# Optimization experiments

Measured on AMD Instinct MI355X. Metric: run time of the kernel, lower is better.

Reference implementation:

```python
import jax, jax.numpy as jnp
import numpy as np

B, S, I, E, NH, HID, L = 32, 512, 64, 128, 8, 1024, 4
HD = E // NH
TEMP = 0.05
EPS_BN = 1e-5
EPS_LN = 1e-5


def _pe(seq_len, d_model):
    # sinusoidal positional encoding, matches PositionalEncoding buffer pe[:seq_len, 0, :]
    pos = jnp.arange(seq_len, dtype=jnp.float32)[:, None]
    div = jnp.exp(jnp.arange(0, d_model, 2, dtype=jnp.float32) * (-np.log(10000.0) / d_model))
    pe = jnp.zeros((seq_len, d_model), jnp.float32)
    pe = pe.at[:, 0::2].set(jnp.sin(pos * div))
    pe = pe.at[:, 1::2].set(jnp.cos(pos * div))
    return pe


def _bn(x, g, b, axis):
    # eval-mode BatchNorm1d with running_mean=0, running_var=1 (affine scale+shift)
    sh = [1] * x.ndim
    sh[axis] = -1
    return x * (g / jnp.sqrt(1.0 + EPS_BN)).reshape(sh) + b.reshape(sh)


def _ln(x, g, b):
    m = jnp.mean(x, axis=-1, keepdims=True)
    v = jnp.var(x, axis=-1, keepdims=True)
    return (x - m) / jnp.sqrt(v + EPS_LN) * g + b


def _layer(h, Wqkv, bqkv, Wo, bo, g1, b1, g2, b2, W1, bf1, W2, bf2):
    # h: (S, B, E); post-LN torch TransformerEncoderLayer, relu FFN
    s, b = h.shape[0], h.shape[1]
    qkv = h @ Wqkv + bqkv                                  # (S, B, 3E)
    q, k, v = jnp.split(qkv, 3, axis=-1)
    sp = lambda t: t.reshape(s, b, NH, HD).transpose(1, 2, 0, 3)  # (B, NH, S, HD)
    q, k, v = sp(q), sp(k), sp(v)
    att = jax.nn.softmax(jnp.einsum('bhqd,bhkd->bhqk', q, k) * (1.0 / np.sqrt(HD)), axis=-1)
    o = jnp.einsum('bhqk,bhkd->bhqd', att, v).transpose(2, 0, 1, 3).reshape(s, b, E)
    h = _ln(h + o @ Wo + bo, g1, b1)
    ff = jax.nn.relu(h @ W1 + bf1) @ W2 + bf2
    h = _ln(h + ff, g2, b2)
    return h, att.mean(axis=1)  # attn averaged over heads: (B, S, S)


def setup_inputs() -> dict:
    key = jax.random.key(0)
    ks = iter(jax.random.split(key, 64))
    r = lambda *sh: jax.random.normal(next(ks), sh, jnp.float32) * 0.02
    return dict(
        x=jax.random.normal(next(ks), (B, S, I), jnp.float32),
        Wt=r(I, E), bt=r(E),
        bn1_g=jnp.ones(E), bn1_b=jnp.zeros(E),
        bn2_g=jnp.ones(E), bn2_b=jnp.zeros(E),
        Wqkv=r(L, E, 3 * E), bqkv=r(L, 3 * E), Wo=r(L, E, E), bo=r(L, E),
        ln1_g=jnp.ones((L, E)), ln1_b=jnp.zeros((L, E)),
        ln2_g=jnp.ones((L, E)), ln2_b=jnp.zeros((L, E)),
        W1=r(L, E, HID), b1=r(L, HID), W2=r(L, HID, E), b2=r(L, E),
        bn3_g=jnp.ones(E), bn3_b=jnp.zeros(E),
        Wd=r(E, I), bd=r(I), bn4_g=jnp.ones(I), bn4_b=jnp.zeros(I),
        Ws=r(S, HID), bs=r(HID), bn5_g=jnp.ones(HID), bn5_b=jnp.zeros(HID),
        Wtext=r(1024, HID), btext=r(HID), lnT_g=jnp.ones(HID), lnT_b=jnp.zeros(HID),
        sensor_emb=jax.random.normal(next(ks), (I, 1024), jnp.float32),
    )


def reference(x, Wt, bt, bn1_g, bn1_b, bn2_g, bn2_b,
              Wqkv, bqkv, Wo, bo, ln1_g, ln1_b, ln2_g, ln2_b,
              W1, b1, W2, b2, bn3_g, bn3_b,
              Wd, bd, bn4_g, bn4_b, Ws, bs, bn5_g, bn5_b,
              Wtext, btext, lnT_g, lnT_b, sensor_emb):
    # trunk_net: Linear -> BN(E) -> PE -> BN(E)
    h = x @ Wt + bt                                  # (B, S, E)
    h = _bn(h.transpose(0, 2, 1), bn1_g, bn1_b, 1)   # (B, E, S)
    h = h.transpose(2, 0, 1)                         # (S, B, E)
    h = h + _pe(h.shape[0], E)[:, None, :]
    h = _bn(h.transpose(1, 2, 0), bn2_g, bn2_b, 1)   # (B, E, S)
    h = h.transpose(2, 0, 1)                         # (S, B, E)
    for i in range(L):
        h, attn = _layer(h, Wqkv[i], bqkv[i], Wo[i], bo[i],
                         ln1_g[i], ln1_b[i], ln2_g[i], ln2_b[i],
                         W1[i], b1[i], W2[i], b2[i])
    h = _bn(h.transpose(1, 2, 0), bn3_g, bn3_b, 1)   # (B, E, S)
    # downsample_embedding_to_input_net
    d = jax.nn.relu(h.transpose(0, 2, 1) @ Wd + bd)  # (B, S, I)
    d = _bn(d.transpose(0, 2, 1), bn4_g, bn4_b, 1)   # (B, I, S)
    # sequence_representation_net
    imu = jax.nn.relu(d @ Ws + bs)                   # (B, I, HID)
    imu = _bn(imu, bn5_g, bn5_b, 2)
    # text_to_shared_net on sensor embeddings
    sens = _ln(jax.nn.relu(sensor_emb @ Wtext + btext), lnT_g, lnT_b)  # (I, HID)
    # fused pairwise cosine similarity (torch expands to (B,I,I,HID); we don't)
    imu_n = imu / jnp.maximum(jnp.linalg.norm(imu, axis=-1, keepdims=True), 1e-8)
    sens_n = sens / jnp.maximum(jnp.linalg.norm(sens, axis=-1, keepdims=True), 1e-8)
    return jnp.einsum('bih,jh->bij', imu_n, sens_n) / TEMP  # (B, I, I)
```

## Files before the change

kernel.cpp:

```cpp
#include <hip/hip_runtime.h>
#include <hip/hip_bf16.h>

#define B_   32
#define S_   512
#define I_   64
#define E_   128
#define NH_  8
#define HD_  16
#define HID_ 1024
#define L_   4
#define NTOK (B_*S_)

typedef __hip_bfloat16 bf16;
typedef __attribute__((ext_vector_type(8))) short bf16x8;
typedef __attribute__((ext_vector_type(4))) float f32x4;

__device__ __forceinline__ float b2f(bf16 v) { return __bfloat162float(v); }

template<bool F32>
__device__ __forceinline__ float ld(const void* p, size_t i) {
    if (F32) return ((const float*)p)[i];
    return b2f(((const bf16*)p)[i]);
}

__device__ __forceinline__ unsigned short f2bu(float f) {
    union { bf16 h; unsigned short u; } c; c.h = __float2bfloat16(f); return c.u;
}
__device__ __forceinline__ unsigned short b2u(bf16 h) {
    union { bf16 h; unsigned short u; } c; c.h = h; return c.u;
}

__global__ void k_flag(const void* bn1g, int* flag) {
    if (threadIdx.x == 0) {
        const unsigned short* u = (const unsigned short*)bn1g;
        int zeros = 0;
        for (int i = 0; i < 32; ++i) zeros += (u[i] == 0);
        flag[0] = (zeros >= 8) ? 1 : 0;
    }
}

template<bool F32>
__device__ void tr_body(const void* in, bf16* __restrict__ out, int R, int C,
                        float (*tile)[33])
{
    size_t off = (size_t)blockIdx.z * R * C;
    int c0 = blockIdx.x * 32, r0 = blockIdx.y * 32;
    int tx = threadIdx.x;
    for (int i = threadIdx.y; i < 32; i += 8)
        tile[i][tx] = ld<F32>(in, off + (size_t)(r0 + i) * C + c0 + tx);
    __syncthreads();
    for (int i = threadIdx.y; i < 32; i += 8)
        out[off + (size_t)(c0 + i) * R + r0 + tx] = __float2bfloat16(tile[tx][i]);
}
__global__ __launch_bounds__(256) void k_tr(
    const void* in, bf16* out, int R, int C, const int* flag)
{
    __shared__ float tile[32][33];
    if (*flag) tr_body<true>(in, out, R, C, tile);
    else       tr_body<false>(in, out, R, C, tile);
}

template<bool F32>
__device__ void trunk_body(const void* x, const void* Wt, const void* bt,
                           const void* g1, const void* c1,
                           const void* g2, const void* c2, float* __restrict__ h,
                           float (*xs)[I_])
{
    const int TOK = 8;
    int t0 = blockIdx.x * TOK;
    int tid = threadIdx.x;
    for (int idx = tid; idx < TOK * I_; idx += 128) {
        int tt = idx >> 6, k = idx & 63;
        xs[tt][k] = ld<F32>(x, (size_t)(t0 + tt) * I_ + k);
    }
    __syncthreads();
    int e = tid;
    float acc[TOK];
    float bias = ld<F32>(bt, e);
#pragma unroll
    for (int tt = 0; tt < TOK; ++tt) acc[tt] = bias;
    for (int k = 0; k < I_; ++k) {
        float w = ld<F32>(Wt, k * E_ + e);
#pragma unroll
        for (int tt = 0; tt < TOK; ++tt) acc[tt] += xs[tt][k] * w;
    }
    float rs = rsqrtf(1.0f + 1e-5f);
    float a1 = ld<F32>(g1, e) * rs, d1 = ld<F32>(c1, e);
    float a2 = ld<F32>(g2, e) * rs, d2 = ld<F32>(c2, e);
    int p = e >> 1;
    float freq = __expf(-(float)p * 0.14391157f);
#pragma unroll
    for (int tt = 0; tt < TOK; ++tt) {
        int t = t0 + tt;
        int s = t & (S_ - 1);
        float ang = (float)s * freq;
        float pe = (e & 1) ? cosf(ang) : sinf(ang);
        float v = acc[tt] * a1 + d1 + pe;
        h[(size_t)t * E_ + e] = v * a2 + d2;
    }
}
__global__ __launch_bounds__(128) void k_trunk(
    const void* x, const void* Wt, const void* bt,
    const void* g1, const void* c1, const void* g2, const void* c2,
    float* h, const int* flag)
{
    __shared__ float xs[8][I_];
    if (*flag) trunk_body<true>(x, Wt, bt, g1, c1, g2, c2, h, xs);
    else       trunk_body<false>(x, Wt, bt, g1, c1, g2, c2, h, xs);
}

template<bool F32>
__device__ void qkvm_body(const float* __restrict__ h, const bf16* __restrict__ WT,
                          const void* bias, size_t obi, bf16* __restrict__ qkv,
                          unsigned short (*A_s)[136])
{
    int t0 = blockIdx.x * 32;
    int tid = threadIdx.x;
    int wv = tid >> 6, lane = tid & 63;
    int l15 = lane & 15, quad = lane >> 4;

    {
        const float4* h4 = (const float4*)(h + (size_t)t0 * E_);
        for (int i = tid; i < 32 * E_ / 4; i += 256) {
            float4 v = h4[i];
            int row = i >> 5, col = (i & 31) * 4;
            A_s[row][col + 0] = f2bu(v.x);
            A_s[row][col + 1] = f2bu(v.y);
            A_s[row][col + 2] = f2bu(v.z);
            A_s[row][col + 3] = f2bu(v.w);
        }
    }
    __syncthreads();

    bf16x8 af[2][4];
#pragma unroll
    for (int kt = 0; kt < 4; ++kt) {
        int k0 = kt * 32 + quad * 8;
        af[0][kt] = *(const bf16x8*)&A_s[l15][k0];
        af[1][kt] = *(const bf16x8*)&A_s[16 + l15][k0];
    }
    for (int nt = 0; nt < 6; ++nt) {
        int col = wv * 96 + nt * 16 + l15;
        f32x4 acc0 = {0.f, 0.f, 0.f, 0.f}, acc1 = {0.f, 0.f, 0.f, 0.f};
#pragma unroll
        for (int kt = 0; kt < 4; ++kt) {
            bf16x8 bfr = *(const bf16x8*)&WT[(size_t)col * E_ + kt * 32 + quad * 8];
            acc0 = __builtin_amdgcn_mfma_f32_16x16x32_bf16(af[0][kt], bfr, acc0, 0, 0, 0);
            acc1 = __builtin_amdgcn_mfma_f32_16x16x32_bf16(af[1][kt], bfr, acc1, 0, 0, 0);
        }
        float bb = ld<F32>(bias, obi + col);
#pragma unroll
        for (int r = 0; r < 4; ++r) {
            qkv[(size_t)(t0 + quad * 4 + r) * 384 + col]      = __float2bfloat16(acc0[r] + bb);
            qkv[(size_t)(t0 + 16 + quad * 4 + r) * 384 + col] = __float2bfloat16(acc1[r] + bb);
        }
    }
}
__global__ __launch_bounds__(256) void k_qkv(
    const float* h, const bf16* WT, const void* bias, size_t obi,
    bf16* qkv, const int* flag)
{
    __shared__ unsigned short A_s[32][136];
    if (*flag) qkvm_body<true>(h, WT, bias, obi, qkv, A_s);
    else       qkvm_body<false>(h, WT, bias, obi, qkv, A_s);
}

__global__ __launch_bounds__(256) void k_attn(bf16* qkv)
{
    __shared__ unsigned short Qs[64 * 24];
    __shared__ unsigned short Ks[S_ * 24];
    __shared__ unsigned short VT[HD_ * 520];
    __shared__ unsigned short Pb[4][16 * 40];

    int bx = blockIdx.x;
    int qg = bx & 7;
    int hh = (bx >> 3) & (NH_ - 1);
    int b  = bx >> 6;
    int tid = threadIdx.x;
    const size_t base = (size_t)(b * S_) * 384 + hh * HD_;
    const float qscale = 0.25f * 1.44269504f;

    for (int i = tid; i < S_ * 8; i += 256) {
        int d2 = i & 7, s = i >> 3;
        const bf16* row = qkv + base + (size_t)s * 384;
        unsigned int uk = (unsigned int)b2u(row[128 + 2 * d2])
                        | ((unsigned int)b2u(row[128 + 2 * d2 + 1]) << 16);
        ((unsigned int*)Ks)[s * 12 + d2] = uk;
    }
    for (int i = tid; i < 64 * 8; i += 256) {
        int d2 = i & 7, s = i >> 3;
        const bf16* row = qkv + base + (size_t)(qg * 64 + s) * 384;
        unsigned int uq = (unsigned int)f2bu(b2f(row[2 * d2]) * qscale)
                        | ((unsigned int)f2bu(b2f(row[2 * d2 + 1]) * qscale) << 16);
        ((unsigned int*)Qs)[s * 12 + d2] = uq;
    }
    for (int i = tid; i < HD_ * (S_ / 2); i += 256) {
        int d = i & 15, s2 = i >> 4;
        unsigned int uv = (unsigned int)b2u(qkv[base + (size_t)(2 * s2) * 384 + 256 + d])
                        | ((unsigned int)b2u(qkv[base + (size_t)(2 * s2 + 1) * 384 + 256 + d]) << 16);
        ((unsigned int*)VT)[d * 260 + s2] = uv;
    }
    __syncthreads();

    int wv = tid >> 6, lane = tid & 63;
    int l15 = lane & 15, quad = lane >> 4;
    bool loquad = (quad < 2);
    unsigned short* Pw = &Pb[wv][0];
    const f32x4 z4 = {0.f, 0.f, 0.f, 0.f};

    bf16x8 B1 = {0, 0, 0, 0, 0, 0, 0, 0};
    if (loquad) B1 = *(const bf16x8*)&Qs[(wv * 16 + l15) * 24 + quad * 8];

    float den = 0.f;
    f32x4 O = z4;

    for (int kt2 = 0; kt2 < 16; ++kt2) {
        int key0 = kt2 * 32;
        bf16x8 A1a = {0, 0, 0, 0, 0, 0, 0, 0};
        bf16x8 A1b = {0, 0, 0, 0, 0, 0, 0, 0};
        if (loquad) {
            A1a = *(const bf16x8*)&Ks[(key0 + l15) * 24 + quad * 8];
            A1b = *(const bf16x8*)&Ks[(key0 + 16 + l15) * 24 + quad * 8];
        }
        f32x4 S1 = __builtin_amdgcn_mfma_f32_16x16x32_bf16(A1a, B1, z4, 0, 0, 0);
        f32x4 S2 = __builtin_amdgcn_mfma_f32_16x16x32_bf16(A1b, B1, z4, 0, 0, 0);

        float p[8];
#pragma unroll
        for (int r = 0; r < 4; ++r) { p[r] = exp2f(S1[r]); den += p[r]; }
#pragma unroll
        for (int r = 0; r < 4; ++r) { p[4 + r] = exp2f(S2[r]); den += p[4 + r]; }

        unsigned int w0 = (unsigned int)f2bu(p[0]) | ((unsigned int)f2bu(p[1]) << 16);
        unsigned int w1 = (unsigned int)f2bu(p[2]) | ((unsigned int)f2bu(p[3]) << 16);
        *(uint2*)&Pw[l15 * 40 + quad * 4] = (uint2){w0, w1};
        unsigned int w2 = (unsigned int)f2bu(p[4]) | ((unsigned int)f2bu(p[5]) << 16);
        unsigned int w3 = (unsigned int)f2bu(p[6]) | ((unsigned int)f2bu(p[7]) << 16);
        *(uint2*)&Pw[l15 * 40 + 16 + quad * 4] = (uint2){w2, w3};

        bf16x8 A2 = *(const bf16x8*)&Pw[l15 * 40 + quad * 8];
        bf16x8 B2 = *(const bf16x8*)&VT[l15 * 520 + key0 + quad * 8];
        O = __builtin_amdgcn_mfma_f32_16x16x32_bf16(A2, B2, O, 0, 0, 0);
    }

    den += __shfl_xor(den, 16, 64);
    den += __shfl_xor(den, 32, 64);
    float inv = 1.0f / den;
    int q0 = qg * 64 + wv * 16;
#pragma unroll
    for (int r = 0; r < 4; ++r) {
        float oi = O[r] * __shfl(inv, quad * 4 + r, 64);
        qkv[(size_t)(b * S_ + q0 + quad * 4 + r) * 384 + hh * HD_ + l15] =
            __float2bfloat16(oi);
    }
}

template<bool F32>
__device__ void projm_body(const bf16* __restrict__ qkv, const bf16* __restrict__ WoT,
                           const void* bo, size_t obo,
                           const void* g, const void* be, size_t oln,
                           float* __restrict__ h,
                           unsigned short (*A_s)[136], float (*red)[32][2])
{
    int t0 = blockIdx.x * 32;
    int tid = threadIdx.x;
    int wv = tid >> 6, lane = tid & 63;
    int l15 = lane & 15, quad = lane >> 4;

    for (int i = tid; i < 32 * 16; i += 256) {
        int row = i >> 4, seg = i & 15;
        *(uint4*)&A_s[row][seg * 8] =
            *(const uint4*)&qkv[(size_t)(t0 + row) * 384 + seg * 8];
    }
    __syncthreads();

    bf16x8 af[2][4];
#pragma unroll
    for (int kt = 0; kt < 4; ++kt) {
        int k0 = kt * 32 + quad * 8;
        af[0][kt] = *(const bf16x8*)&A_s[l15][k0];
        af[1][kt] = *(const bf16x8*)&A_s[16 + l15][k0];
    }
    f32x4 acc[2][2];
#pragma unroll
    for (int a = 0; a < 2; ++a)
#pragma unroll
        for (int bn = 0; bn < 2; ++bn) acc[a][bn] = (f32x4){0.f, 0.f, 0.f, 0.f};
    int c0 = wv * 32 + l15, c1 = c0 + 16;
#pragma unroll
    for (int kt = 0; kt < 4; ++kt) {
        int k0 = kt * 32 + quad * 8;
        bf16x8 bb0 = *(const bf16x8*)&WoT[(size_t)c0 * E_ + k0];
        bf16x8 bb1 = *(const bf16x8*)&WoT[(size_t)c1 * E_ + k0];
        acc[0][0] = __builtin_amdgcn_mfma_f32_16x16x32_bf16(af[0][kt], bb0, acc[0][0], 0, 0, 0);
        acc[1][0] = __builtin_amdgcn_mfma_f32_16x16x32_bf16(af[1][kt], bb0, acc[1][0], 0, 0, 0);
        acc[0][1] = __builtin_amdgcn_mfma_f32_16x16x32_bf16(af[0][kt], bb1, acc[0][1], 0, 0, 0);
        acc[1][1] = __builtin_amdgcn_mfma_f32_16x16x32_bf16(af[1][kt], bb1, acc[1][1], 0, 0, 0);
    }

    float bo0 = ld<F32>(bo, obo + c0), bo1 = ld<F32>(bo, obo + c1);
    float val[2][2][4], s1[2][4], s2[2][4];
#pragma unroll
    for (int mt = 0; mt < 2; ++mt) {
#pragma unroll
        for (int r = 0; r < 4; ++r) {
            size_t row = (size_t)(t0 + mt * 16 + quad * 4 + r);
            float v0 = acc[mt][0][r] + bo0 + h[row * E_ + c0];
            float v1 = acc[mt][1][r] + bo1 + h[row * E_ + c1];
            val[mt][0][r] = v0; val[mt][1][r] = v1;
            s1[mt][r] = v0 + v1;
            s2[mt][r] = v0 * v0 + v1 * v1;
        }
    }
#pragma unroll
    for (int off = 1; off < 16; off <<= 1) {
#pragma unroll
        for (int mt = 0; mt < 2; ++mt)
#pragma unroll
            for (int r = 0; r < 4; ++r) {
                s1[mt][r] += __shfl_xor(s1[mt][r], off, 64);
                s2[mt][r] += __shfl_xor(s2[mt][r], off, 64);
            }
    }
    if (l15 == 0) {
#pragma unroll
        for (int mt = 0; mt < 2; ++mt)
#pragma unroll
            for (int r = 0; r < 4; ++r) {
                red[wv][mt * 16 + quad * 4 + r][0] = s1[mt][r];
                red[wv][mt * 16 + quad * 4 + r][1] = s2[mt][r];
            }
    }
    __syncthreads();
    float g0 = ld<F32>(g, oln + c0), g1v = ld<F32>(g, oln + c1);
    float be0 = ld<F32>(be, oln + c0), be1 = ld<F32>(be, oln + c1);
#pragma unroll
    for (int mt = 0; mt < 2; ++mt) {
#pragma unroll
        for (int r = 0; r < 4; ++r) {
            int rw = mt * 16 + quad * 4 + r;
            float su = red[0][rw][0] + red[1][rw][0] + red[2][rw][0] + red[3][rw][0];
            float sq = red[0][rw][1] + red[1][rw][1] + red[2][rw][1] + red[3][rw][1];
            float mean = su * (1.0f / E_);
            float var = fmaxf(sq * (1.0f / E_) - mean * mean, 0.0f);
            float rstd = rsqrtf(var + 1e-5f);
            size_t row = (size_t)(t0 + rw);
            h[row * E_ + c0] = (val[mt][0][r] - mean) * rstd * g0 + be0;
            h[row * E_ + c1] = (val[mt][1][r] - mean) * rstd * g1v + be1;
        }
    }
}
__global__ __launch_bounds__(256) void k_proj(
    const bf16* qkv, const bf16* WoT, const void* bo, size_t obo,
    const void* g, const void* be, size_t oln, float* h, const int* flag)
{
    __shared__ unsigned short A_s[32][136];
    __shared__ float red[4][32][2];
    if (*flag) projm_body<true>(qkv, WoT, bo, obo, g, be, oln, h, A_s, red);
    else       projm_body<false>(qkv, WoT, bo, obo, g, be, oln, h, A_s, red);
}

#define FTOK 32
#define APAD 8
#define MPAD 8

template<bool F32>
__device__ void ffn_body(float* __restrict__ h,
                         const bf16* __restrict__ W1T, const void* b1, size_t ob1,
                         const bf16* __restrict__ W2T, const void* b2v, size_t ob2,
                         const void* g, const void* be, size_t oln,
                         unsigned short (*A_s)[E_ + APAD],
                         unsigned short (*mid_s)[HID_ + MPAD],
                         float (*red)[32][2])
{
    int t0 = blockIdx.x * FTOK;
    int tid = threadIdx.x;
    int wv = tid >> 6, lane = tid & 63;
    int l15 = lane & 15, quad = lane >> 4;

    {
        const float4* h4 = (const float4*)(h + (size_t)t0 * E_);
        for (int i = tid; i < FTOK * E_ / 4; i += 256) {
            float4 v = h4[i];
            int row = i >> 5, col = (i & 31) * 4;
            A_s[row][col + 0] = f2bu(v.x);
            A_s[row][col + 1] = f2bu(v.y);
            A_s[row][col + 2] = f2bu(v.z);
            A_s[row][col + 3] = f2bu(v.w);
        }
    }
    __syncthreads();

    {
        bf16x8 af[2][4];
#pragma unroll
        for (int kt = 0; kt < 4; ++kt) {
            int k0 = kt * 32 + quad * 8;
            af[0][kt] = *(const bf16x8*)&A_s[l15][k0];
            af[1][kt] = *(const bf16x8*)&A_s[16 + l15][k0];
        }
        for (int nt = 0; nt < 16; ++nt) {
            int col = wv * 256 + nt * 16 + l15;
            f32x4 acc0 = {0.f, 0.f, 0.f, 0.f}, acc1 = {0.f, 0.f, 0.f, 0.f};
#pragma unroll
            for (int kt = 0; kt < 4; ++kt) {
                bf16x8 bfr = *(const bf16x8*)&W1T[(size_t)col * E_ + kt * 32 + quad * 8];
                acc0 = __builtin_amdgcn_mfma_f32_16x16x32_bf16(af[0][kt], bfr, acc0, 0, 0, 0);
                acc1 = __builtin_amdgcn_mfma_f32_16x16x32_bf16(af[1][kt], bfr, acc1, 0, 0, 0);
            }
            float bias = ld<F32>(b1, ob1 + col);
#pragma unroll
            for (int r = 0; r < 4; ++r) {
                mid_s[quad * 4 + r][col]      = f2bu(fmaxf(acc0[r] + bias, 0.f));
                mid_s[16 + quad * 4 + r][col] = f2bu(fmaxf(acc1[r] + bias, 0.f));
            }
        }
    }
    __syncthreads();

    f32x4 acc[2][2];
#pragma unroll
    for (int a = 0; a < 2; ++a)
#pragma unroll
        for (int bn = 0; bn < 2; ++bn) acc[a][bn] = (f32x4){0.f, 0.f, 0.f, 0.f};
    int c0 = wv * 32 + l15;
    int c1 = wv * 32 + 16 + l15;
    for (int kt = 0; kt < 32; ++kt) {
        int k0 = kt * 32 + quad * 8;
        bf16x8 a0 = *(const bf16x8*)&mid_s[l15][k0];
        bf16x8 a1 = *(const bf16x8*)&mid_s[16 + l15][k0];
        bf16x8 bb0 = *(const bf16x8*)&W2T[(size_t)c0 * HID_ + k0];
        bf16x8 bb1 = *(const bf16x8*)&W2T[(size_t)c1 * HID_ + k0];
        acc[0][0] = __builtin_amdgcn_mfma_f32_16x16x32_bf16(a0, bb0, acc[0][0], 0, 0, 0);
        acc[1][0] = __builtin_amdgcn_mfma_f32_16x16x32_bf16(a1, bb0, acc[1][0], 0, 0, 0);
        acc[0][1] = __builtin_amdgcn_mfma_f32_16x16x32_bf16(a0, bb1, acc[0][1], 0, 0, 0);
        acc[1][1] = __builtin_amdgcn_mfma_f32_16x16x32_bf16(a1, bb1, acc[1][1], 0, 0, 0);
    }

    float bo0 = ld<F32>(b2v, ob2 + c0), bo1 = ld<F32>(b2v, ob2 + c1);
    float val[2][2][4], s1[2][4], s2[2][4];
#pragma unroll
    for (int mt = 0; mt < 2; ++mt) {
#pragma unroll
        for (int r = 0; r < 4; ++r) {
            size_t row = (size_t)(t0 + mt * 16 + quad * 4 + r);
            float v0 = acc[mt][0][r] + bo0 + h[row * E_ + c0];
            float v1 = acc[mt][1][r] + bo1 + h[row * E_ + c1];
            val[mt][0][r] = v0; val[mt][1][r] = v1;
            s1[mt][r] = v0 + v1;
            s2[mt][r] = v0 * v0 + v1 * v1;
        }
    }
#pragma unroll
    for (int off = 1; off < 16; off <<= 1) {
#pragma unroll
        for (int mt = 0; mt < 2; ++mt)
#pragma unroll
            for (int r = 0; r < 4; ++r) {
                s1[mt][r] += __shfl_xor(s1[mt][r], off, 64);
                s2[mt][r] += __shfl_xor(s2[mt][r], off, 64);
            }
    }
    if (l15 == 0) {
#pragma unroll
        for (int mt = 0; mt < 2; ++mt)
#pragma unroll
            for (int r = 0; r < 4; ++r) {
                red[wv][mt * 16 + quad * 4 + r][0] = s1[mt][r];
                red[wv][mt * 16 + quad * 4 + r][1] = s2[mt][r];
            }
    }
    __syncthreads();
    float g0 = ld<F32>(g, oln + c0), g1v = ld<F32>(g, oln + c1);
    float be0 = ld<F32>(be, oln + c0), be1 = ld<F32>(be, oln + c1);
#pragma unroll
    for (int mt = 0; mt < 2; ++mt) {
#pragma unroll
        for (int r = 0; r < 4; ++r) {
            int rw = mt * 16 + quad * 4 + r;
            float su = red[0][rw][0] + red[1][rw][0] + red[2][rw][0] + red[3][rw][0];
            float sq = red[0][rw][1] + red[1][rw][1] + red[2][rw][1] + red[3][rw][1];
            float mean = su * (1.0f / E_);
            float var = fmaxf(sq * (1.0f / E_) - mean * mean, 0.0f);
            float rstd = rsqrtf(var + 1e-5f);
            size_t row = (size_t)(t0 + rw);
            h[row * E_ + c0] = (val[mt][0][r] - mean) * rstd * g0 + be0;
            h[row * E_ + c1] = (val[mt][1][r] - mean) * rstd * g1v + be1;
        }
    }
}
__global__ __launch_bounds__(256) void k_ffn_mfma(
    float* h, const bf16* W1T, const void* b1, size_t ob1,
    const bf16* W2T, const void* b2v, size_t ob2,
    const void* g, const void* be, size_t oln, const int* flag)
{
    __shared__ unsigned short A_s[FTOK][E_ + APAD];
    __shared__ unsigned short mid_s[FTOK][HID_ + MPAD];
    __shared__ float red[4][32][2];
    if (*flag) ffn_body<true>(h, W1T, b1, ob1, W2T, b2v, ob2, g, be, oln, A_s, mid_s, red);
    else       ffn_body<false>(h, W1T, b1, ob1, W2T, b2v, ob2, g, be, oln, A_s, mid_s, red);
}

template<bool F32>
__device__ void downm_body(const float* __restrict__ h, const void* g3, const void* c3,
                           const bf16* __restrict__ WdT, const void* bd,
                           const void* g4, const void* c4, float* __restrict__ d,
                           unsigned short (*A_s)[136], float* g3s, float* c3s)
{
    int t0 = blockIdx.x * 32;
    int tid = threadIdx.x;
    if (tid < E_) {
        float rs = rsqrtf(1.0f + 1e-5f);
        g3s[tid] = ld<F32>(g3, tid) * rs;
        c3s[tid] = ld<F32>(c3, tid);
    }
    __syncthreads();
    for (int i = tid; i < 32 * E_; i += 256) {
        int row = i >> 7, col = i & 127;
        A_s[row][col] = f2bu(h[(size_t)(t0 + row) * E_ + col] * g3s[col] + c3s[col]);
    }
    __syncthreads();

    int wv = tid >> 6, lane = tid & 63;
    int l15 = lane & 15, quad = lane >> 4;
    int col = wv * 16 + l15;
    f32x4 acc0 = {0.f, 0.f, 0.f, 0.f}, acc1 = {0.f, 0.f, 0.f, 0.f};
#pragma unroll
    for (int kt = 0; kt < 4; ++kt) {
        int k0 = kt * 32 + quad * 8;
        bf16x8 a0 = *(const bf16x8*)&A_s[l15][k0];
        bf16x8 a1 = *(const bf16x8*)&A_s[16 + l15][k0];
        bf16x8 bb = *(const bf16x8*)&WdT[(size_t)col * E_ + k0];
        acc0 = __builtin_amdgcn_mfma_f32_16x16x32_bf16(a0, bb, acc0, 0, 0, 0);
        acc1 = __builtin_amdgcn_mfma_f32_16x16x32_bf16(a1, bb, acc1, 0, 0, 0);
    }
    float rs = rsqrtf(1.0f + 1e-5f);
    float bb = ld<F32>(bd, col);
    float a4 = ld<F32>(g4, col) * rs, d4 = ld<F32>(c4, col);
#pragma unroll
    for (int r = 0; r < 4; ++r) {
        d[(size_t)(t0 + quad * 4 + r) * I_ + col]      = fmaxf(acc0[r] + bb, 0.f) * a4 + d4;
        d[(size_t)(t0 + 16 + quad * 4 + r) * I_ + col] = fmaxf(acc1[r] + bb, 0.f) * a4 + d4;
    }
}
__global__ __launch_bounds__(256) void k_down(
    const float* h, const void* g3, const void* c3, const bf16* WdT, const void* bd,
    const void* g4, const void* c4, float* d, const int* flag)
{
    __shared__ unsigned short A_s[32][136];
    __shared__ float g3s[E_], c3s[E_];
    if (*flag) downm_body<true>(h, g3, c3, WdT, bd, g4, c4, d, A_s, g3s, c3s);
    else       downm_body<false>(h, g3, c3, WdT, bd, g4, c4, d, A_s, g3s, c3s);
}

template<bool F32>
__device__ void imum_body(const float* __restrict__ d, const bf16* __restrict__ WsT,
                          const void* bs, const void* g5, const void* c5,
                          float* __restrict__ imu, unsigned short (*A_s)[520])
{
    int b = blockIdx.x >> 3;
    int jc = blockIdx.x & 7;
    int tid = threadIdx.x;
    int wv = tid >> 6, lane = tid & 63;
    int l15 = lane & 15, quad = lane >> 4;

    for (int idx = tid; idx < I_ * S_; idx += 256) {
        int i = idx & 63, s = idx >> 6;
        A_s[i][s] = f2bu(d[((size_t)b * S_ + s) * I_ + i]);
    }
    __syncthreads();

    float rs = rsqrtf(1.0f + 1e-5f);
    int j0 = jc * 128 + wv * 32;
    for (int nt = 0; nt < 2; ++nt) {
        int j = j0 + nt * 16 + l15;
        f32x4 acc4[4];
#pragma unroll
        for (int mt = 0; mt < 4; ++mt) acc4[mt] = (f32x4){0.f, 0.f, 0.f, 0.f};
        for (int kt = 0; kt < 16; ++kt) {
            int k0 = kt * 32 + quad * 8;
            bf16x8 bfr = *(const bf16x8*)&WsT[(size_t)j * S_ + k0];
#pragma unroll
            for (int mt = 0; mt < 4; ++mt) {
                bf16x8 a = *(const bf16x8*)&A_s[mt * 16 + l15][k0];
                acc4[mt] = __builtin_amdgcn_mfma_f32_16x16x32_bf16(a, bfr, acc4[mt], 0, 0, 0);
            }
        }
        float bias = ld<F32>(bs, j);
        float a5 = ld<F32>(g5, j) * rs, d5 = ld<F32>(c5, j);
#pragma unroll
        for (int mt = 0; mt < 4; ++mt) {
#pragma unroll
            for (int r = 0; r < 4; ++r) {
                int row = mt * 16 + quad * 4 + r;
                float v = fmaxf(acc4[mt][r] + bias, 0.f) * a5 + d5;
                imu[((size_t)b * I_ + row) * HID_ + j] = v;
            }
        }
    }
}
__global__ __launch_bounds__(256) void k_imu(
    const float* d, const bf16* WsT, const void* bs,
    const void* g5, const void* c5, float* imu, const int* flag)
{
    __shared__ unsigned short A_s[I_][520];
    if (*flag) imum_body<true>(d, WsT, bs, g5, c5, imu, A_s);
    else       imum_body<false>(d, WsT, bs, g5, c5, imu, A_s);
}

__global__ __launch_bounds__(256) void k_norm(float* __restrict__ imu)
{
    __shared__ float red[4];
    size_t r0 = (size_t)blockIdx.x * HID_;
    int tid = threadIdx.x;
    float sq = 0.f;
    for (int k = tid; k < HID_; k += 256) { float v = imu[r0 + k]; sq += v * v; }
    for (int off = 32; off; off >>= 1) sq += __shfl_down(sq, off, 64);
    int wv = tid >> 6, lane = tid & 63;
    if (lane == 0) red[wv] = sq;
    __syncthreads();
    float tot = red[0] + red[1] + red[2] + red[3];
    float inv = 1.0f / fmaxf(sqrtf(fmaxf(tot, 0.f)), 1e-8f);
    for (int k = tid; k < HID_; k += 256) imu[r0 + k] *= inv;
}

template<bool F32>
__device__ void sensg_body(const void* se, const bf16* __restrict__ WtT,
                           const void* bt, float* __restrict__ sg,
                           unsigned short (*A_s)[HID_ + 8])
{
    int mt = blockIdx.x >> 4;
    int nc = blockIdx.x & 15;
    int r0 = mt * 16;
    int tid = threadIdx.x;
    int wv = tid >> 6, lane = tid & 63;
    int l15 = lane & 15, quad = lane >> 4;

    for (int i = tid; i < 16 * HID_; i += 256) {
        int row = i >> 10, col = i & (HID_ - 1);
        A_s[row][col] = f2bu(ld<F32>(se, (size_t)(r0 + row) * HID_ + col));
    }
    __syncthreads();

    int col = nc * 64 + wv * 16 + l15;
    f32x4 acc = {0.f, 0.f, 0.f, 0.f};
    for (int kt = 0; kt < 32; ++kt) {
        int k0 = kt * 32 + quad * 8;
        bf16x8 a = *(const bf16x8*)&A_s[l15][k0];
        bf16x8 bb = *(const bf16x8*)&WtT[(size_t)col * HID_ + k0];
        acc = __builtin_amdgcn_mfma_f32_16x16x32_bf16(a, bb, acc, 0, 0, 0);
    }
    float bbv = ld<F32>(bt, col);
#pragma unroll
    for (int r = 0; r < 4; ++r)
        sg[(size_t)(r0 + quad * 4 + r) * HID_ + col] = fmaxf(acc[r] + bbv, 0.f);
}
__global__ __launch_bounds__(256) void k_sens_gemm(
    const void* se, const bf16* WtT, const void* bt, float* sg, const int* flag)
{
    __shared__ unsigned short A_s[16][HID_ + 8];
    if (*flag) sensg_body<true>(se, WtT, bt, sg, A_s);
    else       sensg_body<false>(se, WtT, bt, sg, A_s);
}

template<bool F32>
__device__ void sensln_body(const float* __restrict__ sg, const void* g, const void* be,
                            bf16* __restrict__ sens_b, float (*red)[2])
{
    size_t r0 = (size_t)blockIdx.x * HID_;
    int tid = threadIdx.x;
    int wv = tid >> 6, lane = tid & 63;
    float v4[4];
    float s1 = 0.f, s2 = 0.f;
#pragma unroll
    for (int c = 0; c < 4; ++c) {
        float v = sg[r0 + tid + c * 256];
        v4[c] = v;
        s1 += v; s2 += v * v;
    }
    for (int off = 32; off; off >>= 1) {
        s1 += __shfl_down(s1, off, 64);
        s2 += __shfl_down(s2, off, 64);
    }
    if (lane == 0) { red[wv][0] = s1; red[wv][1] = s2; }
    __syncthreads();
    float su = red[0][0] + red[1][0] + red[2][0] + red[3][0];
    float sq = red[0][1] + red[1][1] + red[2][1] + red[3][1];
    float mean = su * (1.0f / HID_);
    float var = fmaxf(sq * (1.0f / HID_) - mean * mean, 0.0f);
    float rstd = rsqrtf(var + 1e-5f);
    float q = 0.f;
#pragma unroll
    for (int c = 0; c < 4; ++c) {
        int col = tid + c * 256;
        v4[c] = (v4[c] - mean) * rstd * ld<F32>(g, col) + ld<F32>(be, col);
        q += v4[c] * v4[c];
    }
    for (int off = 32; off; off >>= 1) q += __shfl_down(q, off, 64);
    __syncthreads();
    if (lane == 0) red[wv][0] = q;
    __syncthreads();
    float tot = red[0][0] + red[1][0] + red[2][0] + red[3][0];
    float inv = 1.0f / fmaxf(sqrtf(fmaxf(tot, 0.f)), 1e-8f);
#pragma unroll
    for (int c = 0; c < 4; ++c)
        sens_b[r0 + tid + c * 256] = __float2bfloat16(v4[c] * inv);
}
__global__ __launch_bounds__(256) void k_sens_ln(
    const float* sg, const void* g, const void* be, bf16* sens_b, const int* flag)
{
    __shared__ float red[4][2];
    if (*flag) sensln_body<true>(sg, g, be, sens_b, red);
    else       sensln_body<false>(sg, g, be, sens_b, red);
}

template<bool F32>
__device__ void finalm_body(const float* __restrict__ imu_n, const bf16* __restrict__ sens_b,
                            void* __restrict__ out, unsigned short (*A_s)[HID_ + 8])
{
    int r0 = blockIdx.x * 32;
    int tid = threadIdx.x;
    int wv = tid >> 6, lane = tid & 63;
    int l15 = lane & 15, quad = lane >> 4;

    {
        const float4* i4 = (const float4*)(imu_n + (size_t)r0 * HID_);
        for (int i = tid; i < 32 * HID_ / 4; i += 256) {
            float4 v = i4[i];
            int row = i >> 8, col = (i & 255) * 4;
            A_s[row][col + 0] = f2bu(v.x);
            A_s[row][col + 1] = f2bu(v.y);
            A_s[row][col + 2] = f2bu(v.z);
            A_s[row][col + 3] = f2bu(v.w);
        }
    }
    __syncthreads();

    int j = wv * 16 + l15;
    f32x4 acc[2];
    acc[0] = (f32x4){0.f, 0.f, 0.f, 0.f};
    acc[1] = (f32x4){0.f, 0.f, 0.f, 0.f};
    for (int kt = 0; kt < 32; ++kt) {
        int k0 = kt * 32 + quad * 8;
        bf16x8 bfr = *(const bf16x8*)&sens_b[(size_t)j * HID_ + k0];
        bf16x8 a0 = *(const bf16x8*)&A_s[l15][k0];
        bf16x8 a1 = *(const bf16x8*)&A_s[16 + l15][k0];
        acc[0] = __builtin_amdgcn_mfma_f32_16x16x32_bf16(a0, bfr, acc[0], 0, 0, 0);
        acc[1] = __builtin_amdgcn_mfma_f32_16x16x32_bf16(a1, bfr, acc[1], 0, 0, 0);
    }
#pragma unroll
    for (int mt = 0; mt < 2; ++mt) {
#pragma unroll
        for (int r = 0; r < 4; ++r) {
            size_t row = (size_t)(r0 + mt * 16 + quad * 4 + r);
            float v = acc[mt][r] * 20.0f;
            if (F32) ((float*)out)[row * I_ + j] = v;
            else     ((bf16*)out)[row * I_ + j] = __float2bfloat16(v);
        }
    }
}
__global__ __launch_bounds__(256) void k_final(
    const float* imu_n, const bf16* sens_b, void* out, const int* flag)
{
    __shared__ unsigned short A_s[32][HID_ + 8];
    if (*flag) finalm_body<true>(imu_n, sens_b, out, A_s);
    else       finalm_body<false>(imu_n, sens_b, out, A_s);
}

extern "C" void kernel_launch(void* const* d_in, const int* in_sizes, int n_in,
                              void* d_out, int out_size, void* d_ws, size_t ws_size,
                              hipStream_t stream) {
    (void)in_sizes; (void)n_in; (void)out_size; (void)ws_size;
    const void* x      = d_in[0];
    const void* Wt     = d_in[1];
    const void* bt     = d_in[2];
    const void* bn1_g  = d_in[3];
    const void* bn1_b  = d_in[4];
    const void* bn2_g  = d_in[5];
    const void* bn2_b  = d_in[6];
    const void* Wqkv   = d_in[7];
    const void* bqkv   = d_in[8];
    const void* Wo     = d_in[9];
    const void* bo     = d_in[10];
    const void* ln1_g  = d_in[11];
    const void* ln1_b  = d_in[12];
    const void* ln2_g  = d_in[13];
    const void* ln2_b  = d_in[14];
    const void* W1     = d_in[15];
    const void* b1     = d_in[16];
    const void* W2     = d_in[17];
    const void* b2     = d_in[18];
    const void* bn3_g  = d_in[19];
    const void* bn3_b  = d_in[20];
    const void* Wd     = d_in[21];
    const void* bd     = d_in[22];
    const void* bn4_g  = d_in[23];
    const void* bn4_b  = d_in[24];
    const void* Wsr    = d_in[25];
    const void* bs     = d_in[26];
    const void* bn5_g  = d_in[27];
    const void* bn5_b  = d_in[28];
    const void* Wtext  = d_in[29];
    const void* btext  = d_in[30];
    const void* lnT_g  = d_in[31];
    const void* lnT_b  = d_in[32];
    const void* semb   = d_in[33];

    char* ws = (char*)d_ws;
    float* h    = (float*)(ws);
    bf16*  qkvb = (bf16*) (ws + ((size_t)8  << 20));
    float* dbuf = (float*)(ws + ((size_t)8  << 20));
    float* imu  = (float*)(ws + ((size_t)12 << 20));
    bf16*  wb   = (bf16*) (ws + ((size_t)20 << 20));
    bf16*  WqkvT = wb;
    bf16*  WoT   = wb + 196608;
    bf16*  W1T   = wb + 262144;
    bf16*  W2T   = wb + 786432;
    bf16*  WsT   = wb + 1310720;
    bf16*  sensb = wb + 1835008;
    bf16*  WdT   = wb + 1900544;
    float* sg    = (float*)(wb + 1908736);
    bf16*  WtxT  = (bf16*)ws;
    int*   flag  = (int*)  (ws + ((size_t)24 << 20));

    k_flag<<<1, 64, 0, stream>>>(bn1_g, flag);

    {
        dim3 blk(32, 8);
        k_tr<<<dim3(384/32, 128/32, L_), blk, 0, stream>>>(Wqkv, WqkvT, 128, 384, flag);
        k_tr<<<dim3(128/32, 128/32, L_), blk, 0, stream>>>(Wo,   WoT,   128, 128, flag);
        k_tr<<<dim3(1024/32, 128/32, L_), blk, 0, stream>>>(W1,  W1T,   128, 1024, flag);
        k_tr<<<dim3(128/32, 1024/32, L_), blk, 0, stream>>>(W2,  W2T,   1024, 128, flag);
        k_tr<<<dim3(1024/32, 512/32, 1), blk, 0, stream>>>(Wsr,  WsT,   512, 1024, flag);
        k_tr<<<dim3(64/32, 128/32, 1),   blk, 0, stream>>>(Wd,   WdT,   128, 64,  flag);
    }

    k_trunk<<<NTOK / 8, 128, 0, stream>>>(x, Wt, bt, bn1_g, bn1_b, bn2_g, bn2_b, h, flag);

    for (int l = 0; l < L_; ++l) {
        size_t obqkv = (size_t)l * 384;
        size_t obo   = (size_t)l * E_;
        size_t ob1   = (size_t)l * HID_;
        size_t ob2   = (size_t)l * E_;
        size_t oln   = (size_t)l * E_;
        k_qkv<<<NTOK / 32, 256, 0, stream>>>(h, WqkvT + (size_t)l * 49152,
                                             bqkv, obqkv, qkvb, flag);
        k_attn<<<B_ * NH_ * 8, 256, 0, stream>>>(qkvb);
        k_proj<<<NTOK / 32, 256, 0, stream>>>(qkvb, WoT + (size_t)l * 16384,
                                              bo, obo, ln1_g, ln1_b, oln, h, flag);
        k_ffn_mfma<<<NTOK / FTOK, 256, 0, stream>>>(h, W1T + (size_t)l * 131072, b1, ob1,
                                                    W2T + (size_t)l * 131072, b2, ob2,
                                                    ln2_g, ln2_b, oln, flag);
    }

    k_down<<<NTOK / 32, 256, 0, stream>>>(h, bn3_g, bn3_b, WdT, bd, bn4_g, bn4_b, dbuf, flag);
    {
        dim3 blk(32, 8);
        k_tr<<<dim3(1024/32, 1024/32, 1), blk, 0, stream>>>(Wtext, WtxT, 1024, 1024, flag);
    }
    k_imu<<<B_ * 8, 256, 0, stream>>>(dbuf, WsT, bs, bn5_g, bn5_b, imu, flag);
    k_norm<<<B_ * I_, 256, 0, stream>>>(imu);
    k_sens_gemm<<<64, 256, 0, stream>>>(semb, WtxT, btext, sg, flag);
    k_sens_ln<<<I_, 256, 0, stream>>>(sg, lnT_g, lnT_b, sensb, flag);
    k_final<<<(B_ * I_) / 32, 256, 0, stream>>>(imu, sensb, d_out, flag);
}
```

Measured before the change: 566.2 us.

## Fuse next-layer QKV projection into FFN epilogue and enlarge attention blocks

The FFN kernel now writes its LayerNorm output into shared memory as bf16 and, for every layer except the last, computes the next layer's QKV projection in place. This removes three k_qkv launches and the re-read of h from global memory. Separately, the attention kernel now handles 128 queries per block with 512 threads instead of 64 with 256. That halves how often K and V are reloaded and transposed into LDS per head, at the cost of more LDS per block and fewer blocks. The FFN kernel gains extra MFMA work and global weight reads in its tail, which may lengthen it.

```diff
diff --git a/kernel.cpp b/kernel.cpp
--- a/kernel.cpp
+++ b/kernel.cpp
@@ -165,36 +165,36 @@
     else       qkvm_body<false>(h, WT, bias, obi, qkv, A_s);
 }
 
-__global__ __launch_bounds__(256) void k_attn(bf16* qkv)
-{
-    __shared__ unsigned short Qs[64 * 24];
+__global__ __launch_bounds__(512) void k_attn(bf16* qkv)
+{
+    __shared__ unsigned short Qs[128 * 24];
     __shared__ unsigned short Ks[S_ * 24];
     __shared__ unsigned short VT[HD_ * 520];
-    __shared__ unsigned short Pb[4][16 * 40];
+    __shared__ unsigned short Pb[8][16 * 40];
 
     int bx = blockIdx.x;
-    int qg = bx & 7;
-    int hh = (bx >> 3) & (NH_ - 1);
-    int b  = bx >> 6;
+    int qg = bx & 3;
+    int hh = (bx >> 2) & (NH_ - 1);
+    int b  = bx >> 5;
     int tid = threadIdx.x;
     const size_t base = (size_t)(b * S_) * 384 + hh * HD_;
     const float qscale = 0.25f * 1.44269504f;
 
-    for (int i = tid; i < S_ * 8; i += 256) {
+    for (int i = tid; i < S_ * 8; i += 512) {
         int d2 = i & 7, s = i >> 3;
         const bf16* row = qkv + base + (size_t)s * 384;
         unsigned int uk = (unsigned int)b2u(row[128 + 2 * d2])
                         | ((unsigned int)b2u(row[128 + 2 * d2 + 1]) << 16);
         ((unsigned int*)Ks)[s * 12 + d2] = uk;
     }
-    for (int i = tid; i < 64 * 8; i += 256) {
+    for (int i = tid; i < 128 * 8; i += 512) {
         int d2 = i & 7, s = i >> 3;
-        const bf16* row = qkv + base + (size_t)(qg * 64 + s) * 384;
+        const bf16* row = qkv + base + (size_t)(qg * 128 + s) * 384;
         unsigned int uq = (unsigned int)f2bu(b2f(row[2 * d2]) * qscale)
                         | ((unsigned int)f2bu(b2f(row[2 * d2 + 1]) * qscale) << 16);
         ((unsigned int*)Qs)[s * 12 + d2] = uq;
     }
-    for (int i = tid; i < HD_ * (S_ / 2); i += 256) {
+    for (int i = tid; i < HD_ * (S_ / 2); i += 512) {
         int d = i & 15, s2 = i >> 4;
         unsigned int uv = (unsigned int)b2u(qkv[base + (size_t)(2 * s2) * 384 + 256 + d])
                         | ((unsigned int)b2u(qkv[base + (size_t)(2 * s2 + 1) * 384 + 256 + d]) << 16);
@@ -246,7 +246,7 @@
     den += __shfl_xor(den, 16, 64);
     den += __shfl_xor(den, 32, 64);
     float inv = 1.0f / den;
-    int q0 = qg * 64 + wv * 16;
+    int q0 = qg * 128 + wv * 16;
 #pragma unroll
     for (int r = 0; r < 4; ++r) {
         float oi = O[r] * __shfl(inv, quad * 4 + r, 64);
@@ -369,6 +369,8 @@
                          const bf16* __restrict__ W1T, const void* b1, size_t ob1,
                          const bf16* __restrict__ W2T, const void* b2v, size_t ob2,
                          const void* g, const void* be, size_t oln,
+                         const bf16* __restrict__ WqkvTn, const void* bqkvp,
+                         size_t obqn, bf16* __restrict__ qkvout,
                          unsigned short (*A_s)[E_ + APAD],
                          unsigned short (*mid_s)[HID_ + MPAD],
                          float (*red)[32][2])
@@ -484,21 +486,56 @@
             float var = fmaxf(sq * (1.0f / E_) - mean * mean, 0.0f);
             float rstd = rsqrtf(var + 1e-5f);
             size_t row = (size_t)(t0 + rw);
-            h[row * E_ + c0] = (val[mt][0][r] - mean) * rstd * g0 + be0;
-            h[row * E_ + c1] = (val[mt][1][r] - mean) * rstd * g1v + be1;
+            float h0 = (val[mt][0][r] - mean) * rstd * g0 + be0;
+            float h1 = (val[mt][1][r] - mean) * rstd * g1v + be1;
+            h[row * E_ + c0] = h0;
+            h[row * E_ + c1] = h1;
+            A_s[rw][c0] = f2bu(h0);
+            A_s[rw][c1] = f2bu(h1);
+        }
+    }
+    __syncthreads();
+
+    if (WqkvTn != nullptr) {
+        bf16x8 af[2][4];
+#pragma unroll
+        for (int kt = 0; kt < 4; ++kt) {
+            int k0 = kt * 32 + quad * 8;
+            af[0][kt] = *(const bf16x8*)&A_s[l15][k0];
+            af[1][kt] = *(const bf16x8*)&A_s[16 + l15][k0];
+        }
+        for (int nt = 0; nt < 6; ++nt) {
+            int col = wv * 96 + nt * 16 + l15;
+            f32x4 q0 = {0.f, 0.f, 0.f, 0.f}, q1 = {0.f, 0.f, 0.f, 0.f};
+#pragma unroll
+            for (int kt = 0; kt < 4; ++kt) {
+                bf16x8 bfr = *(const bf16x8*)&WqkvTn[(size_t)col * E_ + kt * 32 + quad * 8];
+                q0 = __builtin_amdgcn_mfma_f32_16x16x32_bf16(af[0][kt], bfr, q0, 0, 0, 0);
+                q1 = __builtin_amdgcn_mfma_f32_16x16x32_bf16(af[1][kt], bfr, q1, 0, 0, 0);
+            }
+            float bb = ld<F32>(bqkvp, obqn + col);
+#pragma unroll
+            for (int r = 0; r < 4; ++r) {
+                qkvout[(size_t)(t0 + quad * 4 + r) * 384 + col]      = __float2bfloat16(q0[r] + bb);
+                qkvout[(size_t)(t0 + 16 + quad * 4 + r) * 384 + col] = __float2bfloat16(q1[r] + bb);
+            }
         }
     }
 }
 __global__ __launch_bounds__(256) void k_ffn_mfma(
     float* h, const bf16* W1T, const void* b1, size_t ob1,
     const bf16* W2T, const void* b2v, size_t ob2,
-    const void* g, const void* be, size_t oln, const int* flag)
+    const void* g, const void* be, size_t oln,
+    const bf16* WqkvTn, const void* bqkvp, size_t obqn, bf16* qkvout,
+    const int* flag)
 {
     __shared__ unsigned short A_s[FTOK][E_ + APAD];
     __shared__ unsigned short mid_s[FTOK][HID_ + MPAD];
     __shared__ float red[4][32][2];
-    if (*flag) ffn_body<true>(h, W1T, b1, ob1, W2T, b2v, ob2, g, be, oln, A_s, mid_s, red);
-    else       ffn_body<false>(h, W1T, b1, ob1, W2T, b2v, ob2, g, be, oln, A_s, mid_s, red);
+    if (*flag) ffn_body<true>(h, W1T, b1, ob1, W2T, b2v, ob2, g, be, oln,
+                              WqkvTn, bqkvp, obqn, qkvout, A_s, mid_s, red);
+    else       ffn_body<false>(h, W1T, b1, ob1, W2T, b2v, ob2, g, be, oln,
+                               WqkvTn, bqkvp, obqn, qkvout, A_s, mid_s, red);
 }
 
 template<bool F32>
@@ -837,20 +874,22 @@
 
     k_trunk<<<NTOK / 8, 128, 0, stream>>>(x, Wt, bt, bn1_g, bn1_b, bn2_g, bn2_b, h, flag);
 
+    k_qkv<<<NTOK / 32, 256, 0, stream>>>(h, WqkvT, bqkv, 0, qkvb, flag);
+
     for (int l = 0; l < L_; ++l) {
-        size_t obqkv = (size_t)l * 384;
         size_t obo   = (size_t)l * E_;
         size_t ob1   = (size_t)l * HID_;
         size_t ob2   = (size_t)l * E_;
         size_t oln   = (size_t)l * E_;
-        k_qkv<<<NTOK / 32, 256, 0, stream>>>(h, WqkvT + (size_t)l * 49152,
-                                             bqkv, obqkv, qkvb, flag);
-        k_attn<<<B_ * NH_ * 8, 256, 0, stream>>>(qkvb);
+        const bf16* WqkvTn = (l + 1 < L_) ? (WqkvT + (size_t)(l + 1) * 49152) : nullptr;
+        size_t obqn = (size_t)(l + 1) * 384;
+        k_attn<<<B_ * NH_ * 4, 512, 0, stream>>>(qkvb);
         k_proj<<<NTOK / 32, 256, 0, stream>>>(qkvb, WoT + (size_t)l * 16384,
                                               bo, obo, ln1_g, ln1_b, oln, h, flag);
         k_ffn_mfma<<<NTOK / FTOK, 256, 0, stream>>>(h, W1T + (size_t)l * 131072, b1, ob1,
                                                     W2T + (size_t)l * 131072, b2, ob2,
-                                                    ln2_g, ln2_b, oln, flag);
+                                                    ln2_g, ln2_b, oln,
+                                                    WqkvTn, bqkv, obqn, qkvb, flag);
     }
 
     k_down<<<NTOK / 32, 256, 0, stream>>>(h, bn3_g, bn3_b, WdT, bd, bn4_g, bn4_b, dbuf, flag);
```

Measured after the change: 578.5 us. 1.02x slower.
